# Optimization experiments

Measured on AMD Instinct MI355X. Metric: run time of the kernel, lower is better.

Reference implementation:

```python
import jax, jax.numpy as jnp
import numpy as np

N, C, F_CAT, F_NUM, V = 250000, 32, 16, 16, 64


def setup_inputs() -> dict:
    key = jax.random.key(0)
    k0, k1, k2, k3, k4, k5 = jax.random.split(key, 6)
    X_cat = jax.random.randint(k0, (N, F_CAT), 0, V)
    X_num = jax.random.normal(k1, (N, F_NUM), dtype=jnp.float32)
    class_probs = jax.random.uniform(k2, (C,), dtype=jnp.float32)
    class_probs = class_probs / class_probs.sum()
    # conditional probs are smoothed counts/size_class in fit(); keep them positive
    cat_probs = jax.random.uniform(k3, (C, F_CAT, V), dtype=jnp.float32) * 0.9 + 0.05
    means = jax.random.normal(k4, (C, F_NUM), dtype=jnp.float32)
    stds = jax.random.uniform(k5, (C, F_NUM), dtype=jnp.float32) + 0.5  # keep away from 0
    return {"X_cat": X_cat, "X_num": X_num, "class_probs": class_probs,
            "cat_probs": cat_probs, "means": means, "stds": stds}


def reference(X_cat, X_num, class_probs, cat_probs, means, stds):
    # X_cat: [N, F_cat] int indices; X_num: [N, F_num] float
    # cat_probs: [C, F_cat, V]; means/stds: [C, F_num]; class_probs: [C]
    C_, Fc, _ = cat_probs.shape
    # categorical gather -> [N, C, F_cat]
    ci = jnp.arange(C_)[None, :, None]
    fi = jnp.arange(Fc)[None, None, :]
    gathered = cat_probs[ci, fi, X_cat[:, None, :]]
    cat_term = jnp.prod(gathered, axis=-1)            # [N, C]
    # gaussian likelihood (faithful to module: 1/(2*pi*std^2) * exp(-0.5*z^2))
    pi = jnp.float32(np.pi)
    x = X_num[:, None, :]                             # [N, 1, F_num]
    z = (x - means[None]) / stds[None]
    lik = 1.0 / (2.0 * pi * stds[None] ** 2) * jnp.exp(-0.5 * z ** 2)  # [N, C, F_num]
    num_term = jnp.prod(lik, axis=-1)                 # [N, C]
    pred_probs = class_probs[None, :] * cat_term * num_term
    return jnp.argmax(pred_probs, axis=1)
```

## Files before the change

kernel.cpp:

```cpp
#include <hip/hip_runtime.h>
#include <math.h>

constexpr int kN  = 250000;
constexpr int kC  = 32;
constexpr int kFC = 16;
constexpr int kFN = 16;
constexpr int kV  = 64;
constexpr int kBlock = 1024;


__global__ __launch_bounds__(256) void nbc_prep(
    const float* __restrict__ class_probs,
    const float* __restrict__ means,
    const float* __restrict__ stds,
    float* __restrict__ ws)
{
    const int t = threadIdx.x;
    const float two_pi = 2.0f * (float)M_PI;
    for (int i = t; i < kC * kFN; i += 256) {
        float m  = means[i];
        float s  = stds[i];
        float rs = 1.0f / s;
        ws[32 + 2 * i]     = -0.5f * rs * rs;
        ws[32 + 2 * i + 1] = m * rs * rs;
    }
    if (t < kC) {
        float k = logf(class_probs[t]);
        for (int f = 0; f < kFN; ++f) {
            float s  = stds[t * kFN + f];
            float m  = means[t * kFN + f];
            float rs = 1.0f / s;
            k += logf(1.0f / (two_pi * (s * s)));
            k += -0.5f * (m * rs) * (m * rs);
        }
        ws[t] = k;
    }
}

__global__ __launch_bounds__(kBlock, 4) void nbc_main(
    const int*   __restrict__ X_cat,
    const float* __restrict__ X_num,
    const float* __restrict__ class_probs,
    const float* __restrict__ cat_probs,
    const float* __restrict__ means,
    const float* __restrict__ stds,
    const float* __restrict__ ws,
    int* __restrict__ out)
{
    __shared__ float lcat[kC * kFC * kV];

    const int tid = threadIdx.x;

    {
        const float4* __restrict__ src = reinterpret_cast<const float4*>(cat_probs);
        float4* dst = reinterpret_cast<float4*>(lcat);
        #pragma unroll
        for (int i = 0; i < (kC * kFC * kV / 4) / kBlock; ++i) {
            int j = i * kBlock + tid;
            float4 v = src[j];
            dst[j] = make_float4(logf(v.x), logf(v.y), logf(v.z), logf(v.w));
        }
    }
    __syncthreads();

    const int n = blockIdx.x * kBlock + tid;
    if (n >= kN) return;

    int   idx[kFC];
    float x  [kFN];
    float xx [kFN];
    {
        const int4* p4 = reinterpret_cast<const int4*>(X_cat + (size_t)n * kFC);
        int4 a0 = p4[0], a1 = p4[1], a2 = p4[2], a3 = p4[3];
        idx[0]=a0.x;  idx[1]=a0.y;  idx[2]=a0.z;  idx[3]=a0.w;
        idx[4]=a1.x;  idx[5]=a1.y;  idx[6]=a1.z;  idx[7]=a1.w;
        idx[8]=a2.x;  idx[9]=a2.y;  idx[10]=a2.z; idx[11]=a2.w;
        idx[12]=a3.x; idx[13]=a3.y; idx[14]=a3.z; idx[15]=a3.w;

        const float4* q4 = reinterpret_cast<const float4*>(X_num + (size_t)n * kFN);
        float4 b0 = q4[0], b1 = q4[1], b2 = q4[2], b3 = q4[3];
        x[0]=b0.x;  x[1]=b0.y;  x[2]=b0.z;  x[3]=b0.w;
        x[4]=b1.x;  x[5]=b1.y;  x[6]=b1.z;  x[7]=b1.w;
        x[8]=b2.x;  x[9]=b2.y;  x[10]=b2.z; x[11]=b2.w;
        x[12]=b3.x; x[13]=b3.y; x[14]=b3.z; x[15]=b3.w;
        #pragma unroll
        for (int f = 0; f < kFN; ++f) xx[f] = x[f] * x[f];
    }

    const float*  __restrict__ K = ws;
    const float2* __restrict__ W = reinterpret_cast<const float2*>(ws + 32);

    float best = -INFINITY, second = -INFINITY;
    int   besti = 0;

    #pragma unroll 2
    for (int c = 0; c < kC; ++c) {
        const float* __restrict__ L = lcat + (c << 10);
        float lc = L[idx[0]];
        #pragma unroll
        for (int f = 1; f < kFC; ++f) {
            lc += L[(f << 6) + idx[f]];
        }

        float ga = 0.0f, gb = 0.0f;
        #pragma unroll
        for (int f = 0; f < kFN; ++f) {
            float2 q = W[(c << 4) + f];
            ga = fmaf(xx[f], q.x, ga);
            gb = fmaf(x[f],  q.y, gb);
        }

        float T = (K[c] + lc) + (ga + gb);
        if (T > best)        { second = best; best = T; besti = c; }
        else if (T > second) { second = T; }
    }

    if (best >= -86.0f && (best - second) >= 8.0e-3f) {
        out[n] = besti;
        return;
    }

    const float thr    = (best >= -86.0f) ? (best - 1.6e-2f) : -INFINITY;
    const float two_pi = 2.0f * (float)M_PI;
    float bb = -INFINITY;
    int   bi = 0;

    for (int c = 0; c < kC; ++c) {
        const float* __restrict__ L = lcat + (c << 10);
        float lc = L[idx[0]];
        #pragma unroll
        for (int f = 1; f < kFC; ++f) lc += L[(f << 6) + idx[f]];
        float ga = 0.0f, gb = 0.0f;
        #pragma unroll
        for (int f = 0; f < kFN; ++f) {
            float2 q = W[(c << 4) + f];
            ga = fmaf(xx[f], q.x, ga);
            gb = fmaf(x[f],  q.y, gb);
        }
        float T = (K[c] + lc) + (ga + gb);

        if (T >= thr) {
            const float* __restrict__ row = cat_probs + (size_t)c * (kFC * kV);
            float cat = row[idx[0]];
            #pragma unroll
            for (int f = 1; f < kFC; ++f) {
                cat *= row[(f << 6) + idx[f]];
            }
            float num;
            #pragma unroll
            for (int f = 0; f < kFN; ++f) {
                float m = means[c * kFN + f];
                float s = stds [c * kFN + f];
                float inv = 1.0f / (two_pi * (s * s));
                float z = (x[f] - m) / s;
                float e = expf(-0.5f * (z * z));
                float lik = inv * e;
                num = (f == 0) ? lik : num * lik;
            }
            float pred = (class_probs[c] * cat) * num;
            if (pred > bb) { bb = pred; bi = c; }
        }
    }
    out[n] = bi;
}

extern "C" void kernel_launch(void* const* d_in, const int* in_sizes, int n_in,
                              void* d_out, int out_size, void* d_ws, size_t ws_size,
                              hipStream_t stream) {
    const int*   X_cat       = (const int*)  d_in[0];
    const float* X_num       = (const float*)d_in[1];
    const float* class_probs = (const float*)d_in[2];
    const float* cat_probs   = (const float*)d_in[3];
    const float* means       = (const float*)d_in[4];
    const float* stds        = (const float*)d_in[5];
    int*   out = (int*)d_out;
    float* ws  = (float*)d_ws;

    hipLaunchKernelGGL(nbc_prep, dim3(1), dim3(256), 0, stream,
                       class_probs, means, stds, ws);

    dim3 block(kBlock);
    dim3 grid((kN + kBlock - 1) / kBlock);
    hipLaunchKernelGGL(nbc_main, grid, block, 0, stream,
                       X_cat, X_num, class_probs, cat_probs, means, stds, ws, out);
}
```

Baseline: 138.8 us.

## Transpose log-prob table in LDS to class-contiguous padded rows with vector reads

The shared log-probability table changes from [class][feature*value] to [feature*value][class], with each row padded to 36 floats. Each thread can then gather all 32 class log-probs for a feature with eight 128-bit LDS reads instead of 32 scalar reads. Per-row results are summed into a 32-entry register accumulator. The Gaussian term now uses a centred (x-m)/s form instead of the expanded quadratic, which costs a few more ALU ops but is numerically safer. Input loads are also issued before the table fill so they can overlap with it. The cost is a larger LDS footprint (about 147KB) and more register pressure from the accumulator array.

```diff
diff --git a/kernel.cpp b/kernel.cpp
--- a/kernel.cpp
+++ b/kernel.cpp
@@ -7,6 +7,8 @@
 constexpr int kFN = 16;
 constexpr int kV  = 64;
 constexpr int kBlock = 1024;
+
+constexpr int kRowDw = 36;
 
 
 __global__ __launch_bounds__(256) void nbc_prep(
@@ -18,22 +20,18 @@
     const int t = threadIdx.x;
     const float two_pi = 2.0f * (float)M_PI;
     for (int i = t; i < kC * kFN; i += 256) {
-        float m  = means[i];
-        float s  = stds[i];
-        float rs = 1.0f / s;
-        ws[32 + 2 * i]     = -0.5f * rs * rs;
-        ws[32 + 2 * i + 1] = m * rs * rs;
+        float m = means[i];
+        float s = stds[i];
+        ws[2 * i]     = m;
+        ws[2 * i + 1] = 1.0f / s;
     }
     if (t < kC) {
         float k = logf(class_probs[t]);
         for (int f = 0; f < kFN; ++f) {
-            float s  = stds[t * kFN + f];
-            float m  = means[t * kFN + f];
-            float rs = 1.0f / s;
+            float s = stds[t * kFN + f];
             k += logf(1.0f / (two_pi * (s * s)));
-            k += -0.5f * (m * rs) * (m * rs);
         }
-        ws[t] = k;
+        ws[2 * kC * kFN + t] = k;
     }
 }
 
@@ -47,29 +45,15 @@
     const float* __restrict__ ws,
     int* __restrict__ out)
 {
-    __shared__ float lcat[kC * kFC * kV];
+    __shared__ float lcat[1024 * kRowDw];
 
     const int tid = threadIdx.x;
-
-    {
-        const float4* __restrict__ src = reinterpret_cast<const float4*>(cat_probs);
-        float4* dst = reinterpret_cast<float4*>(lcat);
-        #pragma unroll
-        for (int i = 0; i < (kC * kFC * kV / 4) / kBlock; ++i) {
-            int j = i * kBlock + tid;
-            float4 v = src[j];
-            dst[j] = make_float4(logf(v.x), logf(v.y), logf(v.z), logf(v.w));
-        }
-    }
-    __syncthreads();
-
-    const int n = blockIdx.x * kBlock + tid;
-    if (n >= kN) return;
+    const int n   = blockIdx.x * kBlock + tid;
+    const bool active = (n < kN);
 
     int   idx[kFC];
     float x  [kFN];
-    float xx [kFN];
-    {
+    if (active) {
         const int4* p4 = reinterpret_cast<const int4*>(X_cat + (size_t)n * kFC);
         int4 a0 = p4[0], a1 = p4[1], a2 = p4[2], a3 = p4[3];
         idx[0]=a0.x;  idx[1]=a0.y;  idx[2]=a0.z;  idx[3]=a0.w;
@@ -83,34 +67,60 @@
         x[4]=b1.x;  x[5]=b1.y;  x[6]=b1.z;  x[7]=b1.w;
         x[8]=b2.x;  x[9]=b2.y;  x[10]=b2.z; x[11]=b2.w;
         x[12]=b3.x; x[13]=b3.y; x[14]=b3.z; x[15]=b3.w;
+    } else {
         #pragma unroll
-        for (int f = 0; f < kFN; ++f) xx[f] = x[f] * x[f];
+        for (int f = 0; f < kFC; ++f) { idx[f] = 0; x[f] = 0.0f; }
     }
 
-    const float*  __restrict__ K = ws;
-    const float2* __restrict__ W = reinterpret_cast<const float2*>(ws + 32);
+    {
+        #pragma unroll
+        for (int cg = 0; cg < 8; ++cg) {
+            float4 w;
+            w.x = logf(cat_probs[(size_t)(cg * 4 + 0) * 1024 + tid]);
+            w.y = logf(cat_probs[(size_t)(cg * 4 + 1) * 1024 + tid]);
+            w.z = logf(cat_probs[(size_t)(cg * 4 + 2) * 1024 + tid]);
+            w.w = logf(cat_probs[(size_t)(cg * 4 + 3) * 1024 + tid]);
+            *reinterpret_cast<float4*>(lcat + (size_t)tid * kRowDw + cg * 4) = w;
+        }
+    }
+    __syncthreads();
+
+    if (!active) return;
+
+    const float2* __restrict__ P = reinterpret_cast<const float2*>(ws);
+    const float*  __restrict__ K = ws + 2 * kC * kFN;
+
+    float acc[kC];
+    #pragma unroll
+    for (int c = 0; c < kC; ++c) acc[c] = 0.0f;
+
+    #pragma unroll
+    for (int f = 0; f < kFC; ++f) {
+        const float4* __restrict__ R = reinterpret_cast<const float4*>(
+            lcat + (size_t)((f << 6) + idx[f]) * kRowDw);
+        #pragma unroll
+        for (int g = 0; g < 8; ++g) {
+            float4 v = R[g];
+            acc[4 * g + 0] += v.x;
+            acc[4 * g + 1] += v.y;
+            acc[4 * g + 2] += v.z;
+            acc[4 * g + 3] += v.w;
+        }
+    }
 
     float best = -INFINITY, second = -INFINITY;
     int   besti = 0;
 
-    #pragma unroll 2
+    #pragma unroll
     for (int c = 0; c < kC; ++c) {
-        const float* __restrict__ L = lcat + (c << 10);
-        float lc = L[idx[0]];
-        #pragma unroll
-        for (int f = 1; f < kFC; ++f) {
-            lc += L[(f << 6) + idx[f]];
-        }
-
-        float ga = 0.0f, gb = 0.0f;
+        float a = 0.0f;
         #pragma unroll
         for (int f = 0; f < kFN; ++f) {
-            float2 q = W[(c << 4) + f];
-            ga = fmaf(xx[f], q.x, ga);
-            gb = fmaf(x[f],  q.y, gb);
+            float2 p = P[(c << 4) + f];
+            float z = (x[f] - p.x) * p.y;
+            a = fmaf(z * z, -0.5f, a);
         }
-
-        float T = (K[c] + lc) + (ga + gb);
+        float T = (K[c] + acc[c]) + a;
         if (T > best)        { second = best; best = T; besti = c; }
         else if (T > second) { second = T; }
     }
@@ -125,19 +135,16 @@
     float bb = -INFINITY;
     int   bi = 0;
 
+    #pragma unroll 2
     for (int c = 0; c < kC; ++c) {
-        const float* __restrict__ L = lcat + (c << 10);
-        float lc = L[idx[0]];
-        #pragma unroll
-        for (int f = 1; f < kFC; ++f) lc += L[(f << 6) + idx[f]];
-        float ga = 0.0f, gb = 0.0f;
+        float a = 0.0f;
         #pragma unroll
         for (int f = 0; f < kFN; ++f) {
-            float2 q = W[(c << 4) + f];
-            ga = fmaf(xx[f], q.x, ga);
-            gb = fmaf(x[f],  q.y, gb);
+            float2 p = P[(c << 4) + f];
+            float z = (x[f] - p.x) * p.y;
+            a = fmaf(z * z, -0.5f, a);
         }
-        float T = (K[c] + lc) + (ga + gb);
+        float T = (K[c] + acc[c]) + a;
 
         if (T >= thr) {
             const float* __restrict__ row = cat_probs + (size_t)c * (kFC * kV);
```

Result: slower. 368.4 us (+165.4%).
